# Kernel optimization log

Hardware: AMD Instinct MI355X
Metric: run time of the kernel (lower is better)

## Reference

```python
import jax, jax.numpy as jnp
import numpy as np

B = 4; C_IN = 3; HW = 224
D_MODEL = 384; D_INNER = 768; D_STATE = 16; DT_RANK = 24; D_CONV = 4
N_LAYERS = 4; NUM_CLASSES = 1000
EPS = 1e-5


def setup_inputs() -> dict:
    key = jax.random.key(0)
    ks = jax.random.split(key, 12)
    def rn(k, shape, scale=0.02):
        return jax.random.normal(k, shape, jnp.float32) * scale
    inp = {}
    inp["x"] = jax.random.normal(ks[0], (B, C_IN, HW, HW), jnp.float32)
    inp["patch_w"] = rn(ks[1], (D_MODEL, C_IN, 4, 4))
    inp["patch_b"] = jnp.zeros((D_MODEL,), jnp.float32)
    inp["in_proj_w"] = rn(ks[2], (N_LAYERS, 2 * D_INNER, D_MODEL))
    inp["conv_w"] = rn(ks[3], (N_LAYERS, D_INNER, 1, D_CONV))
    inp["conv_b"] = jnp.zeros((N_LAYERS, D_INNER), jnp.float32)
    inp["x_proj_w"] = rn(ks[4], (N_LAYERS, DT_RANK + 2 * D_STATE, D_INNER))
    inp["dt_proj_w"] = rn(ks[5], (N_LAYERS, D_INNER, DT_RANK))
    inp["dt_proj_b"] = rn(ks[6], (N_LAYERS, D_INNER), 0.1)
    A = jnp.tile(jnp.arange(1, D_STATE + 1, dtype=jnp.float32)[None, :], (D_INNER, 1))
    inp["A_log"] = jnp.tile(jnp.log(A)[None], (N_LAYERS, 1, 1))
    inp["Dp"] = jnp.ones((N_LAYERS, D_INNER), jnp.float32)
    inp["out_proj_w"] = rn(ks[7], (N_LAYERS, D_MODEL, D_INNER))
    inp["norm_w"] = jnp.ones((D_MODEL,), jnp.float32)
    inp["head_w"] = rn(ks[8], (NUM_CLASSES, D_MODEL))
    inp["head_b"] = jnp.zeros((NUM_CLASSES,), jnp.float32)
    return inp


def selective_scan(u, delta, A, Bm, Cm, Dv):
    # u, delta: [b,l,d]; A: [d,n]; Bm, Cm: [b,l,n]; Dv: [d]
    dA = jnp.exp(delta[..., None] * A)                 # [b,l,d,n]
    dBu = (delta * u)[..., None] * Bm[:, :, None, :]   # [b,l,d,n]

    def step(h, inp):
        a, bu, c = inp
        h = a * h + bu                                  # [b,d,n]
        y = jnp.einsum('bdn,bn->bd', h, c)
        return h, y

    h0 = jnp.zeros((u.shape[0], u.shape[2], A.shape[1]), u.dtype)
    xs = (jnp.swapaxes(dA, 0, 1), jnp.swapaxes(dBu, 0, 1), jnp.swapaxes(Cm, 0, 1))
    _, ys = jax.lax.scan(step, h0, xs)                  # ys: [l,b,d]
    y = jnp.swapaxes(ys, 0, 1)                          # [b,l,d]
    return y + u * Dv


def mamba_block(x, p):
    xr = x @ p['in_proj_w'].T                           # [b,l,2*d_inner]
    xc, res = jnp.split(xr, 2, axis=-1)
    # depthwise causal conv1d (left pad d_conv-1 == pad both + truncate right)
    xt = jnp.swapaxes(xc, 1, 2)                         # [b,d_inner,l]
    xt = jax.lax.conv_general_dilated(
        xt, p['conv_w'], (1,), [(D_CONV - 1, 0)],
        feature_group_count=D_INNER,
        dimension_numbers=('NCH', 'OIH', 'NCH')) + p['conv_b'][None, :, None]
    xc = jax.nn.silu(jnp.swapaxes(xt, 1, 2))
    # S6
    dbl = xc @ p['x_proj_w'].T                          # [b,l,dt_rank+2n]
    dt, Bm, Cm = jnp.split(dbl, [DT_RANK, DT_RANK + D_STATE], axis=-1)
    delta = jax.nn.softplus(dt @ p['dt_proj_w'].T + p['dt_proj_b'])
    y = selective_scan(xc, delta, -jnp.exp(p['A_log']), Bm, Cm, p['Dp'])
    y = y * jax.nn.silu(res)
    return y @ p['out_proj_w'].T


def reference(x, patch_w, patch_b, in_proj_w, conv_w, conv_b, x_proj_w,
              dt_proj_w, dt_proj_b, A_log, Dp, out_proj_w, norm_w, head_w, head_b):
    h = jax.lax.conv_general_dilated(
        x, patch_w, (4, 4), 'VALID',
        dimension_numbers=('NCHW', 'OIHW', 'NCHW')) + patch_b[None, :, None, None]
    b, d, hh, ww = h.shape
    t = jnp.transpose(h.reshape(b, d, hh * ww), (0, 2, 1))  # [b,l,d_model]
    layer_params = dict(in_proj_w=in_proj_w, conv_w=conv_w, conv_b=conv_b,
                        x_proj_w=x_proj_w, dt_proj_w=dt_proj_w, dt_proj_b=dt_proj_b,
                        A_log=A_log, Dp=Dp, out_proj_w=out_proj_w)
    for i in range(N_LAYERS):
        p = {k: v[i] for k, v in layer_params.items()}
        t = t + mamba_block(t, p)
    rms = jnp.sqrt(jnp.mean(t * t, axis=-1, keepdims=True) + EPS)
    t = t / rms * norm_w
    pooled = t.mean(axis=1)
    return pooled @ head_w.T + head_b
```

## Files before the change

kernel.cpp:

```cpp
#include <hip/hip_runtime.h>
#include <math.h>


namespace {
constexpr int NB = 4;
constexpr int SL = 3136;
constexpr int DM = 384;
constexpr int DI = 768;
constexpr int DSN = 16;
constexpr int DR = 24;
constexpr int NLAYER = 4;
constexpr int NCLS = 1000;
constexpr int XPN = DR + 2 * DSN;
constexpr int NCHAIN = NB * DI;
constexpr int PTOK = 32;
}

typedef float f32x4 __attribute__((ext_vector_type(4)));
typedef short short8 __attribute__((ext_vector_type(8)));
typedef short short4v __attribute__((ext_vector_type(4)));

__device__ __forceinline__ float siluf(float x) { return x / (1.f + expf(-x)); }
__device__ __forceinline__ float softplusf(float x) {
  return fmaxf(x, 0.f) + log1pf(expf(-fabsf(x)));
}
__device__ __forceinline__ unsigned short cvt_bf(float f) {
  unsigned int x = __float_as_uint(f);
  unsigned int r = (x + 0x7fffu + ((x >> 16) & 1u)) >> 16;
  return (unsigned short)r;
}

__global__ __launch_bounds__(128) void k_patch(
    const float* __restrict__ x, const float* __restrict__ w,
    const float* __restrict__ bias, float* __restrict__ t,
    unsigned short* __restrict__ tb) {
  __shared__ float patch[PTOK][48];
  const int tid = threadIdx.x;
  const int m0 = blockIdx.x * PTOK;
  const int b = m0 / SL, lbase = m0 % SL;
#pragma unroll
  for (int i = 0; i < 3; ++i) {
    const int c = tid + i * 128;
    const int tok = c / 12, r = c % 12;
    const int ch = r >> 2, kh = r & 3;
    const int l = lbase + tok;
    const int hh = l / 56, ww = l % 56;
    const float4 v =
        *(const float4*)&x[((size_t)(b * 3 + ch) * 224 + (hh * 4 + kh)) * 224 + ww * 4];
    *(float4*)&patch[tok][ch * 16 + kh * 4] = v;
  }
  __syncthreads();
#pragma unroll 1
  for (int i = 0; i < 3; ++i) {
    const int dm = tid + i * 128;
    float4 wr[12];
    const float4* w4 = (const float4*)(w + (size_t)dm * 48);
#pragma unroll
    for (int q = 0; q < 12; ++q) wr[q] = w4[q];
    const float bv = bias[dm];
#pragma unroll 1
    for (int tok0 = 0; tok0 < PTOK; tok0 += 8) {
      float acc[8];
#pragma unroll
      for (int j = 0; j < 8; ++j) acc[j] = bv;
#pragma unroll
      for (int q = 0; q < 12; ++q) {
        const float4 wv = wr[q];
#pragma unroll
        for (int j = 0; j < 8; ++j) {
          const float4 pv = *(const float4*)&patch[tok0 + j][q * 4];
          acc[j] = fmaf(pv.x, wv.x, acc[j]);
          acc[j] = fmaf(pv.y, wv.y, acc[j]);
          acc[j] = fmaf(pv.z, wv.z, acc[j]);
          acc[j] = fmaf(pv.w, wv.w, acc[j]);
        }
      }
#pragma unroll
      for (int j = 0; j < 8; ++j) {
        const size_t o = ((size_t)(m0 + tok0 + j)) * DM + dm;
        t[o] = acc[j];
        tb[o] = cvt_bf(acc[j]);
      }
    }
  }
}

template <int BM, int BN, int MEPI, int NCAP, bool AT>
__global__ __launch_bounds__(256) void k_mgemm(
    const unsigned short* __restrict__ A, const float* __restrict__ Afp,
    const float* __restrict__ W, float* __restrict__ out,
    float* __restrict__ out2, unsigned short* __restrict__ outb, const int K) {
  constexpr int WM = BM / 2, WN = BN / 2, FM = WM / 16, FN = WN / 16;
  constexpr bool NMASK = (NCAP % BN) != 0;
  __shared__ unsigned short As[BM * 40];
  __shared__ unsigned short Bs[BN * 40];
  const int tid = threadIdx.x;
  const int lane = tid & 63, wave = tid >> 6;
  const int wm = wave >> 1, wn = wave & 1;
  const int m0 = blockIdx.x * BM, n0 = blockIdx.y * BN;
  const int r16 = lane & 15, kg = (lane >> 4) * 8;
  f32x4 acc[FM][FN] = {};
  const int nk = K >> 5;
  for (int kt = 0; kt < nk; ++kt) {
    const int k0 = kt << 5;
    if constexpr (AT) {
#pragma unroll
      for (int it = 0; it < BM / 64; ++it) {
        const int c = tid + 256 * it;
        const int kp = c & 15;
        const int lq = (c >> 4) * 4;
        const int mrow = m0 + lq;
        const int bb = mrow / SL;
        const size_t rowo = (size_t)(bb * K + k0 + 2 * kp) * SL + (mrow - bb * SL);
        const float4 v0 = *(const float4*)&Afp[rowo];
        const float4 v1 = *(const float4*)&Afp[rowo + SL];
        const float ve0[4] = {v0.x, v0.y, v0.z, v0.w};
        const float ve1[4] = {v1.x, v1.y, v1.z, v1.w};
#pragma unroll
        for (int e = 0; e < 4; ++e) {
          const unsigned int pk =
              (unsigned int)cvt_bf(ve0[e]) | ((unsigned int)cvt_bf(ve1[e]) << 16);
          *(unsigned int*)&As[(lq + e) * 40 + 2 * kp] = pk;
        }
      }
    } else {
#pragma unroll
      for (int it = 0; it < (BM * 4) / 256; ++it) {
        const int c = tid + 256 * it;
        const int row = c >> 2, ks = (c & 3) * 8;
        *(short8*)&As[row * 40 + ks] =
            *(const short8*)&A[(size_t)(m0 + row) * K + k0 + ks];
      }
    }
#pragma unroll
    for (int it = 0; it < (BN * 8) / 256; ++it) {
      const int c = tid + 256 * it;
      const int row = c >> 3, ks = (c & 7) * 4;
      float4 v = make_float4(0.f, 0.f, 0.f, 0.f);
      if (!NMASK || (n0 + row) < NCAP)
        v = *(const float4*)&W[(size_t)(n0 + row) * K + k0 + ks];
      short4v o4;
      o4[0] = (short)cvt_bf(v.x);
      o4[1] = (short)cvt_bf(v.y);
      o4[2] = (short)cvt_bf(v.z);
      o4[3] = (short)cvt_bf(v.w);
      *(short4v*)&Bs[row * 40 + ks] = o4;
    }
    __syncthreads();
    short8 af[FM], bfv[FN];
#pragma unroll
    for (int i = 0; i < FM; ++i)
      af[i] = *(const short8*)&As[(wm * WM + i * 16 + r16) * 40 + kg];
#pragma unroll
    for (int j = 0; j < FN; ++j)
      bfv[j] = *(const short8*)&Bs[(wn * WN + j * 16 + r16) * 40 + kg];
#pragma unroll
    for (int i = 0; i < FM; ++i)
#pragma unroll
      for (int j = 0; j < FN; ++j)
        acc[i][j] = __builtin_amdgcn_mfma_f32_16x16x32_bf16(af[i], bfv[j],
                                                            acc[i][j], 0, 0, 0);
    __syncthreads();
  }

#pragma unroll
  for (int i = 0; i < FM; ++i) {
#pragma unroll
    for (int j = 0; j < FN; ++j) {
      const int n = n0 + wn * WN + j * 16 + r16;
      const int mb = m0 + wm * WM + i * 16 + ((lane >> 4) << 2);
      f32x4 a = acc[i][j];
      if (MEPI == 0) {
        if (n < DR) {
#pragma unroll
          for (int r = 0; r < 4; ++r) out[(size_t)(mb + r) * DR + n] = a[r];
        } else if (n < NCAP) {
#pragma unroll
          for (int r = 0; r < 4; ++r) out2[(size_t)(mb + r) * 32 + (n - DR)] = a[r];
        }
      } else if (MEPI == 1) {
        float* base = out;
        int nn = n;
        if (n >= DI) { base = out2; nn = n - DI; }
        const int bb = mb / SL;
        const int ll = mb - bb * SL;
        *(f32x4*)&base[((size_t)(bb * DI + nn)) * SL + ll] = a;
      } else {
#pragma unroll
        for (int r = 0; r < 4; ++r) {
          const size_t off = (size_t)(mb + r) * DM + n;
          const float nv = out[off] + a[r];
          out[off] = nv;
          outb[off] = cvt_bf(nv);
        }
      }
    }
  }
}

template <int EPI, bool KTAIL, int NCAP>
__global__ __launch_bounds__(256) void k_gemm(
    const float* __restrict__ A, const float* __restrict__ W,
    const float* __restrict__ bias, float* __restrict__ out, int K, int lda) {
  __shared__ float sm[4352];
  const int tid = threadIdx.x;
  const int m0 = blockIdx.x * 64;
  const int n0 = blockIdx.y * 64;
  const int b = m0 / SL, l0 = m0 % SL;
  const int tm = tid >> 4, tn = tid & 15;
  float acc[4][4] = {};
  float* As = sm;
  float* Ws = sm + 16 * 68;

  const int nk = (K + 15) / 16;
  for (int kt = 0; kt < nk; ++kt) {
    const int k0 = kt * 16;
    {
      const int row = tid >> 2;
      const int kq = (tid & 3) * 4;
      const int kb = k0 + kq;
      float4 v = make_float4(0.f, 0.f, 0.f, 0.f);
      if (!KTAIL || kb < K) v = *(const float4*)&A[(size_t)(m0 + row) * lda + kb];
      As[(kq + 0) * 68 + row] = v.x;
      As[(kq + 1) * 68 + row] = v.y;
      As[(kq + 2) * 68 + row] = v.z;
      As[(kq + 3) * 68 + row] = v.w;
    }
    {
      const int row = tid >> 2;
      const int kq = (tid & 3) * 4;
      const int kb = k0 + kq;
      float4 v = make_float4(0.f, 0.f, 0.f, 0.f);
      const bool nok = (NCAP % 64 == 0) || (n0 + row < NCAP);
      if (nok && (!KTAIL || kb < K)) v = *(const float4*)&W[(size_t)(n0 + row) * K + kb];
      Ws[(kq + 0) * 68 + row] = v.x;
      Ws[(kq + 1) * 68 + row] = v.y;
      Ws[(kq + 2) * 68 + row] = v.z;
      Ws[(kq + 3) * 68 + row] = v.w;
    }
    __syncthreads();
#pragma unroll
    for (int kk = 0; kk < 16; ++kk) {
      const float4 av = *(const float4*)&As[kk * 68 + 4 * tm];
      const float4 wv = *(const float4*)&Ws[kk * 68 + 4 * tn];
      const float ax[4] = {av.x, av.y, av.z, av.w};
      const float wx[4] = {wv.x, wv.y, wv.z, wv.w};
#pragma unroll
      for (int i = 0; i < 4; ++i)
#pragma unroll
        for (int j = 0; j < 4; ++j) acc[i][j] = fmaf(ax[i], wx[j], acc[i][j]);
    }
    __syncthreads();
  }

#pragma unroll
  for (int j = 0; j < 4; ++j) {
    const int nn = 4 * tn + j;
#pragma unroll
    for (int i = 0; i < 4; ++i) {
      float v = acc[i][j];
      if (EPI == 2) v = softplusf(v + bias[n0 + nn]);
      sm[nn * 68 + 4 * tm + i] = v;
    }
  }
  __syncthreads();
  const int row = tid >> 2;
  const int seg = (tid & 3) * 16;
  const float* src = &sm[row * 68 + seg];
  float* dst = out + ((size_t)(b * DI + n0 + row)) * SL + l0 + seg;
#pragma unroll
  for (int q = 0; q < 4; ++q) {
    *(float4*)&dst[q * 4] = *(const float4*)&src[q * 4];
  }
}

__global__ void k_conv(const float* __restrict__ xcT, const float* __restrict__ cw,
                       const float* __restrict__ cb, float* __restrict__ uT) {
  const size_t idx = (size_t)blockIdx.x * 256 + threadIdx.x;
  const int l4 = (int)(idx % (SL / 4)) * 4;
  const int bd = (int)(idx / (SL / 4));
  const int d = bd % DI;
  const float* row = xcT + (size_t)bd * SL;
  const float4 w = *(const float4*)&cw[d * 4];
  const float4 cur = *(const float4*)&row[l4];
  float p1 = 0.f, p2 = 0.f, p3 = 0.f;
  if (l4 > 0) {
    const float4 pv = *(const float4*)&row[l4 - 4];
    p1 = pv.y; p2 = pv.z; p3 = pv.w;
  }
  const float cbd = cb[d];
  float4 o;
  o.x = cbd + w.w * cur.x + w.z * p3 + w.y * p2 + w.x * p1;
  o.y = cbd + w.w * cur.y + w.z * cur.x + w.y * p3 + w.x * p2;
  o.z = cbd + w.w * cur.z + w.z * cur.y + w.y * cur.x + w.x * p3;
  o.w = cbd + w.w * cur.w + w.z * cur.z + w.y * cur.y + w.x * cur.x;
  o.x = siluf(o.x); o.y = siluf(o.y); o.z = siluf(o.z); o.w = siluf(o.w);
  *(float4*)&uT[(size_t)bd * SL + l4] = o;
}

__global__ __launch_bounds__(256) void k_scanw(
    const float* __restrict__ deltaT, const float* __restrict__ uT,
    const float* __restrict__ BC, const float* __restrict__ resT,
    const float* __restrict__ A_log, const float* __restrict__ Dp,
    float* __restrict__ yT) {
  const int tid = threadIdx.x;
  const int lane = tid & 63, wv = tid >> 6;
  const int n = lane & 15, g = lane >> 4;
  const int chain = blockIdx.x * 4 + wv;
  const int b = chain / DI, d = chain % DI;
  const float a2 = -expf(A_log[d * DSN + n]) * 1.44269504088896341f;
  const float dp = Dp[d];
  const float* drow = deltaT + (size_t)chain * SL;
  const float* urow = uT + (size_t)chain * SL;
  const float* resr = resT + (size_t)chain * SL;
  const float* bcb = BC + (size_t)b * SL * 32;
  float* yr = yT + (size_t)chain * SL;
  float carry = 0.f;
  const bool b0 = n & 1, b1 = (n >> 1) & 1, b2 = (n >> 2) & 1, b3 = (n >> 3) & 1;

  for (int tb = 0; tb < SL; tb += 64) {
    const int l0 = tb + g * 16;
    float da[16], dbu[16];
    float h = 0.f, dsum = 0.f;
#pragma unroll
    for (int k = 0; k < 16; ++k) {
      const float dl = drow[l0 + k];
      const float ul = urow[l0 + k];
      const float Bv = bcb[(size_t)(l0 + k) * 32 + n];
      const float e = exp2f(dl * a2);
      da[k] = e;
      dbu[k] = dl * ul * Bv;
      h = fmaf(e, h, dbu[k]);
      dsum += dl;
    }
    float Aagg = exp2f(a2 * dsum);
    float Bagg = h;
#pragma unroll
    for (int off = 16; off <= 32; off <<= 1) {
      const float Ae = __shfl(Aagg, (lane - off) & 63);
      const float Be = __shfl(Bagg, (lane - off) & 63);
      if (lane >= off) {
        Bagg = fmaf(Aagg, Be, Bagg);
        Aagg *= Ae;
      }
    }
    const float Pa = __shfl(Aagg, (lane - 16) & 63);
    const float Pb = __shfl(Bagg, (lane - 16) & 63);
    const float hstart = (g == 0) ? carry : fmaf(Pa, carry, Pb);
    const float cA = __shfl(Aagg, 48 | n);
    const float cB = __shfl(Bagg, 48 | n);
    float p[16];
    h = hstart;
#pragma unroll
    for (int k = 0; k < 16; ++k) {
      h = fmaf(da[k], h, dbu[k]);
      p[k] = h * bcb[(size_t)(l0 + k) * 32 + 16 + n];
    }
    carry = fmaf(cA, carry, cB);
    float q8[8];
#pragma unroll
    for (int i = 0; i < 8; ++i) {
      const float mine = b0 ? p[2 * i + 1] : p[2 * i];
      const float oth = b0 ? p[2 * i] : p[2 * i + 1];
      q8[i] = mine + __shfl_xor(oth, 1);
    }
    float q4[4];
#pragma unroll
    for (int i = 0; i < 4; ++i) {
      const float mine = b1 ? q8[2 * i + 1] : q8[2 * i];
      const float oth = b1 ? q8[2 * i] : q8[2 * i + 1];
      q4[i] = mine + __shfl_xor(oth, 2);
    }
    float q2[2];
#pragma unroll
    for (int i = 0; i < 2; ++i) {
      const float mine = b2 ? q4[2 * i + 1] : q4[2 * i];
      const float oth = b2 ? q4[2 * i] : q4[2 * i + 1];
      q2[i] = mine + __shfl_xor(oth, 4);
    }
    const float mine = b3 ? q2[1] : q2[0];
    const float oth = b3 ? q2[0] : q2[1];
    const float ysum = mine + __shfl_xor(oth, 8);
    const float ul = urow[l0 + n];
    const float r = resr[l0 + n];
    yr[l0 + n] = (ysum + ul * dp) * siluf(r);
  }
}

__global__ void k_rinv(const float* __restrict__ t, float* __restrict__ rinv) {
  const int row = blockIdx.x;
  const float* tr = t + (size_t)row * DM;
  const int tid = threadIdx.x;
  float ss = 0.f;
#pragma unroll
  for (int k = 0; k < DM / 64; ++k) {
    const float v = tr[tid + k * 64];
    ss = fmaf(v, v, ss);
  }
  ss += __shfl_xor(ss, 1);
  ss += __shfl_xor(ss, 2);
  ss += __shfl_xor(ss, 4);
  ss += __shfl_xor(ss, 8);
  ss += __shfl_xor(ss, 16);
  ss += __shfl_xor(ss, 32);
  if (tid == 0) rinv[row] = 1.f / sqrtf(ss / DM + 1e-5f);
}

__global__ void k_pool(const float* __restrict__ t, const float* __restrict__ rinv,
                       float* __restrict__ part) {
  const int b = blockIdx.x, dmb = blockIdx.y, ch = blockIdx.z;
  const int dm = dmb * 64 + threadIdx.x;
  const int lbeg = ch * (SL / 32);
  float s = 0.f;
  for (int l = lbeg; l < lbeg + SL / 32; ++l)
    s = fmaf(t[((size_t)b * SL + l) * DM + dm], rinv[b * SL + l], s);
  part[((size_t)ch * NB + b) * DM + dm] = s;
}

__global__ void k_head(const float* __restrict__ part, const float* __restrict__ norm_w,
                       const float* __restrict__ hw, const float* __restrict__ hb,
                       float* __restrict__ out) {
  const int b = blockIdx.x;
  const int tid = threadIdx.x;
  __shared__ float pv[DM];
  for (int k = tid; k < DM; k += 64) {
    float s = 0.f;
#pragma unroll
    for (int c = 0; c < 32; ++c) s += part[((size_t)c * NB + b) * DM + k];
    pv[k] = s * norm_w[k] * (1.f / SL);
  }
  __syncthreads();
  const int cls = blockIdx.y * 64 + tid;
  if (cls < NCLS) {
    const float* wr = hw + (size_t)cls * DM;
    float acc = hb[cls];
#pragma unroll 4
    for (int k = 0; k < DM; k += 4) {
      const float4 w4 = *(const float4*)&wr[k];
      acc = fmaf(pv[k], w4.x, acc);
      acc = fmaf(pv[k + 1], w4.y, acc);
      acc = fmaf(pv[k + 2], w4.z, acc);
      acc = fmaf(pv[k + 3], w4.w, acc);
    }
    out[(size_t)b * NCLS + cls] = acc;
  }
}

extern "C" void kernel_launch(void* const* d_in, const int* in_sizes, int n_in,
                              void* d_out, int out_size, void* d_ws, size_t ws_size,
                              hipStream_t stream) {
  (void)in_sizes; (void)n_in; (void)out_size; (void)ws_size;
  const float* x = (const float*)d_in[0];
  const float* patch_w = (const float*)d_in[1];
  const float* patch_b = (const float*)d_in[2];
  const float* in_proj_w = (const float*)d_in[3];
  const float* conv_w = (const float*)d_in[4];
  const float* conv_b = (const float*)d_in[5];
  const float* x_proj_w = (const float*)d_in[6];
  const float* dt_proj_w = (const float*)d_in[7];
  const float* dt_proj_b = (const float*)d_in[8];
  const float* A_log = (const float*)d_in[9];
  const float* Dp = (const float*)d_in[10];
  const float* out_proj_w = (const float*)d_in[11];
  const float* norm_w = (const float*)d_in[12];
  const float* head_w = (const float*)d_in[13];
  const float* head_b = (const float*)d_in[14];

  float* ws = (float*)d_ws;
  size_t o = 0;
  float* t = ws + o;     o += (size_t)NB * SL * DM;
  float* xcT = ws + o;   o += (size_t)NB * DI * SL;
  float* resT = ws + o;  o += (size_t)NB * DI * SL;
  float* uT = ws + o;    o += (size_t)NB * DI * SL;
  float* dltT = ws + o;  o += (size_t)NB * DI * SL;
  float* yT = ws + o;    o += (size_t)NB * DI * SL;
  float* dbl24 = ws + o; o += (size_t)NB * SL * DR;
  float* BC = ws + o;    o += (size_t)NB * SL * 32;
  float* rinv = ws + o;  o += (size_t)NB * SL;
  float* part = ws + o;  o += (size_t)32 * NB * DM;
  unsigned short* tb = (unsigned short*)(ws + o); o += (size_t)NB * SL * DM / 2;

  k_patch<<<(NB * SL) / PTOK, 128, 0, stream>>>(x, patch_w, patch_b, t, tb);

  for (int i = 0; i < NLAYER; ++i) {
    k_mgemm<128, 128, 1, 1536, false><<<dim3(98, 12), 256, 0, stream>>>(
        tb, nullptr, in_proj_w + (size_t)i * 2 * DI * DM, xcT, resT, nullptr, DM);
    k_conv<<<(NB * DI * SL / 4) / 256, 256, 0, stream>>>(
        xcT, conv_w + (size_t)i * DI * 4, conv_b + (size_t)i * DI, uT);
    k_mgemm<64, 64, 0, XPN, true><<<dim3(196, 1), 256, 0, stream>>>(
        nullptr, uT, x_proj_w + (size_t)i * XPN * DI, dbl24, BC, nullptr, DI);
    k_gemm<2, true, 64><<<dim3(196, 12), 256, 0, stream>>>(
        dbl24, dt_proj_w + (size_t)i * DI * DR, dt_proj_b + (size_t)i * DI, dltT,
        DR, DR);
    k_scanw<<<NCHAIN / 4, 256, 0, stream>>>(
        dltT, uT, BC, resT, A_log + (size_t)i * DI * DSN, Dp + (size_t)i * DI, yT);
    k_mgemm<128, 128, 2, 384, true><<<dim3(98, 3), 256, 0, stream>>>(
        nullptr, yT, out_proj_w + (size_t)i * DM * DI, t, nullptr, tb, DI);
  }

  k_rinv<<<NB * SL, 64, 0, stream>>>(t, rinv);
  k_pool<<<dim3(NB, DM / 64, 32), 64, 0, stream>>>(t, rinv, part);
  k_head<<<dim3(NB, 16), 64, 0, stream>>>(part, norm_w, head_w, head_b, (float*)d_out);
}
```

Baseline: 1.176 ms.

## Store intermediate activations xc, res, u, y in bf16 instead of fp32

```diff
diff --git a/kernel.cpp b/kernel.cpp
--- a/kernel.cpp
+++ b/kernel.cpp
@@ -19,6 +19,7 @@
 typedef float f32x4 __attribute__((ext_vector_type(4)));
 typedef short short8 __attribute__((ext_vector_type(8)));
 typedef short short4v __attribute__((ext_vector_type(4)));
+typedef unsigned short us4 __attribute__((ext_vector_type(4)));
 
 __device__ __forceinline__ float siluf(float x) { return x / (1.f + expf(-x)); }
 __device__ __forceinline__ float softplusf(float x) {
@@ -28,6 +29,9 @@
   unsigned int x = __float_as_uint(f);
   unsigned int r = (x + 0x7fffu + ((x >> 16) & 1u)) >> 16;
   return (unsigned short)r;
+}
+__device__ __forceinline__ float bf2f(unsigned short v) {
+  return __uint_as_float((unsigned int)v << 16);
 }
 
 __global__ __launch_bounds__(128) void k_patch(
@@ -87,7 +91,7 @@
 
 template <int BM, int BN, int MEPI, int NCAP, bool AT>
 __global__ __launch_bounds__(256) void k_mgemm(
-    const unsigned short* __restrict__ A, const float* __restrict__ Afp,
+    const unsigned short* __restrict__ A, const unsigned short* __restrict__ Abf,
     const float* __restrict__ W, float* __restrict__ out,
     float* __restrict__ out2, unsigned short* __restrict__ outb, const int K) {
   constexpr int WM = BM / 2, WN = BN / 2, FM = WM / 16, FN = WN / 16;
@@ -112,14 +116,12 @@
         const int mrow = m0 + lq;
         const int bb = mrow / SL;
         const size_t rowo = (size_t)(bb * K + k0 + 2 * kp) * SL + (mrow - bb * SL);
-        const float4 v0 = *(const float4*)&Afp[rowo];
-        const float4 v1 = *(const float4*)&Afp[rowo + SL];
-        const float ve0[4] = {v0.x, v0.y, v0.z, v0.w};
-        const float ve1[4] = {v1.x, v1.y, v1.z, v1.w};
+        const us4 v0 = *(const us4*)&Abf[rowo];
+        const us4 v1 = *(const us4*)&Abf[rowo + SL];
 #pragma unroll
         for (int e = 0; e < 4; ++e) {
           const unsigned int pk =
-              (unsigned int)cvt_bf(ve0[e]) | ((unsigned int)cvt_bf(ve1[e]) << 16);
+              (unsigned int)v0[e] | ((unsigned int)v1[e] << 16);
           *(unsigned int*)&As[(lq + e) * 40 + 2 * kp] = pk;
         }
       }
@@ -179,12 +181,15 @@
           for (int r = 0; r < 4; ++r) out2[(size_t)(mb + r) * 32 + (n - DR)] = a[r];
         }
       } else if (MEPI == 1) {
-        float* base = out;
+        unsigned short* base = (unsigned short*)out;
         int nn = n;
-        if (n >= DI) { base = out2; nn = n - DI; }
+        if (n >= DI) { base = (unsigned short*)out2; nn = n - DI; }
         const int bb = mb / SL;
         const int ll = mb - bb * SL;
-        *(f32x4*)&base[((size_t)(bb * DI + nn)) * SL + ll] = a;
+        us4 o4;
+#pragma unroll
+        for (int r = 0; r < 4; ++r) o4[r] = cvt_bf(a[r]);
+        *(us4*)&base[((size_t)(bb * DI + nn)) * SL + ll] = o4;
       } else {
 #pragma unroll
         for (int r = 0; r < 4; ++r) {
@@ -274,35 +279,40 @@
   }
 }
 
-__global__ void k_conv(const float* __restrict__ xcT, const float* __restrict__ cw,
-                       const float* __restrict__ cb, float* __restrict__ uT) {
+__global__ void k_conv(const unsigned short* __restrict__ xcT,
+                       const float* __restrict__ cw, const float* __restrict__ cb,
+                       unsigned short* __restrict__ uT) {
   const size_t idx = (size_t)blockIdx.x * 256 + threadIdx.x;
   const int l4 = (int)(idx % (SL / 4)) * 4;
   const int bd = (int)(idx / (SL / 4));
   const int d = bd % DI;
-  const float* row = xcT + (size_t)bd * SL;
+  const unsigned short* row = xcT + (size_t)bd * SL;
   const float4 w = *(const float4*)&cw[d * 4];
-  const float4 cur = *(const float4*)&row[l4];
+  const us4 cu = *(const us4*)&row[l4];
+  const float c0 = bf2f(cu[0]), c1 = bf2f(cu[1]), c2 = bf2f(cu[2]), c3 = bf2f(cu[3]);
   float p1 = 0.f, p2 = 0.f, p3 = 0.f;
   if (l4 > 0) {
-    const float4 pv = *(const float4*)&row[l4 - 4];
-    p1 = pv.y; p2 = pv.z; p3 = pv.w;
+    const us4 pv = *(const us4*)&row[l4 - 4];
+    p1 = bf2f(pv[1]); p2 = bf2f(pv[2]); p3 = bf2f(pv[3]);
   }
   const float cbd = cb[d];
-  float4 o;
-  o.x = cbd + w.w * cur.x + w.z * p3 + w.y * p2 + w.x * p1;
-  o.y = cbd + w.w * cur.y + w.z * cur.x + w.y * p3 + w.x * p2;
-  o.z = cbd + w.w * cur.z + w.z * cur.y + w.y * cur.x + w.x * p3;
-  o.w = cbd + w.w * cur.w + w.z * cur.z + w.y * cur.y + w.x * cur.x;
-  o.x = siluf(o.x); o.y = siluf(o.y); o.z = siluf(o.z); o.w = siluf(o.w);
-  *(float4*)&uT[(size_t)bd * SL + l4] = o;
+  float o0 = cbd + w.w * c0 + w.z * p3 + w.y * p2 + w.x * p1;
+  float o1 = cbd + w.w * c1 + w.z * c0 + w.y * p3 + w.x * p2;
+  float o2 = cbd + w.w * c2 + w.z * c1 + w.y * c0 + w.x * p3;
+  float o3 = cbd + w.w * c3 + w.z * c2 + w.y * c1 + w.x * c0;
+  us4 o4;
+  o4[0] = cvt_bf(siluf(o0));
+  o4[1] = cvt_bf(siluf(o1));
+  o4[2] = cvt_bf(siluf(o2));
+  o4[3] = cvt_bf(siluf(o3));
+  *(us4*)&uT[(size_t)bd * SL + l4] = o4;
 }
 
 __global__ __launch_bounds__(256) void k_scanw(
-    const float* __restrict__ deltaT, const float* __restrict__ uT,
-    const float* __restrict__ BC, const float* __restrict__ resT,
+    const float* __restrict__ deltaT, const unsigned short* __restrict__ uT,
+    const float* __restrict__ BC, const unsigned short* __restrict__ resT,
     const float* __restrict__ A_log, const float* __restrict__ Dp,
-    float* __restrict__ yT) {
+    unsigned short* __restrict__ yT) {
   const int tid = threadIdx.x;
   const int lane = tid & 63, wv = tid >> 6;
   const int n = lane & 15, g = lane >> 4;
@@ -311,10 +321,10 @@
   const float a2 = -expf(A_log[d * DSN + n]) * 1.44269504088896341f;
   const float dp = Dp[d];
   const float* drow = deltaT + (size_t)chain * SL;
-  const float* urow = uT + (size_t)chain * SL;
-  const float* resr = resT + (size_t)chain * SL;
+  const unsigned short* urow = uT + (size_t)chain * SL;
+  const unsigned short* resr = resT + (size_t)chain * SL;
   const float* bcb = BC + (size_t)b * SL * 32;
-  float* yr = yT + (size_t)chain * SL;
+  unsigned short* yr = yT + (size_t)chain * SL;
   float carry = 0.f;
   const bool b0 = n & 1, b1 = (n >> 1) & 1, b2 = (n >> 2) & 1, b3 = (n >> 3) & 1;
 
@@ -325,7 +335,7 @@
 #pragma unroll
     for (int k = 0; k < 16; ++k) {
       const float dl = drow[l0 + k];
-      const float ul = urow[l0 + k];
+      const float ul = bf2f(urow[l0 + k]);
       const float Bv = bcb[(size_t)(l0 + k) * 32 + n];
       const float e = exp2f(dl * a2);
       da[k] = e;
@@ -381,9 +391,9 @@
     const float mine = b3 ? q2[1] : q2[0];
     const float oth = b3 ? q2[0] : q2[1];
     const float ysum = mine + __shfl_xor(oth, 8);
-    const float ul = urow[l0 + n];
-    const float r = resr[l0 + n];
-    yr[l0 + n] = (ysum + ul * dp) * siluf(r);
+    const float uln = bf2f(urow[l0 + n]);
+    const float r = bf2f(resr[l0 + n]);
+    yr[l0 + n] = cvt_bf((ysum + uln * dp) * siluf(r));
   }
 }
 
@@ -469,11 +479,11 @@
   float* ws = (float*)d_ws;
   size_t o = 0;
   float* t = ws + o;     o += (size_t)NB * SL * DM;
-  float* xcT = ws + o;   o += (size_t)NB * DI * SL;
-  float* resT = ws + o;  o += (size_t)NB * DI * SL;
-  float* uT = ws + o;    o += (size_t)NB * DI * SL;
+  unsigned short* xcT = (unsigned short*)(ws + o);  o += (size_t)NB * DI * SL / 2;
+  unsigned short* resT = (unsigned short*)(ws + o); o += (size_t)NB * DI * SL / 2;
+  unsigned short* uT = (unsigned short*)(ws + o);   o += (size_t)NB * DI * SL / 2;
+  unsigned short* yT = (unsigned short*)(ws + o);   o += (size_t)NB * DI * SL / 2;
   float* dltT = ws + o;  o += (size_t)NB * DI * SL;
-  float* yT = ws + o;    o += (size_t)NB * DI * SL;
   float* dbl24 = ws + o; o += (size_t)NB * SL * DR;
   float* BC = ws + o;    o += (size_t)NB * SL * 32;
   float* rinv = ws + o;  o += (size_t)NB * SL;
@@ -484,7 +494,8 @@
 
   for (int i = 0; i < NLAYER; ++i) {
     k_mgemm<128, 128, 1, 1536, false><<<dim3(98, 12), 256, 0, stream>>>(
-        tb, nullptr, in_proj_w + (size_t)i * 2 * DI * DM, xcT, resT, nullptr, DM);
+        tb, nullptr, in_proj_w + (size_t)i * 2 * DI * DM, (float*)xcT, (float*)resT,
+        nullptr, DM);
     k_conv<<<(NB * DI * SL / 4) / 256, 256, 0, stream>>>(
         xcT, conv_w + (size_t)i * DI * 4, conv_b + (size_t)i * DI, uT);
     k_mgemm<64, 64, 0, XPN, true><<<dim3(196, 1), 256, 0, stream>>>(
```

Result: faster. 1.137 ms (-3.3%).
